# Kernel optimization log

Measured on AMD Instinct MI355X. Metric: run time of the kernel, lower is better.

The kernel has to match this reference:

```python
import jax, jax.numpy as jnp
import numpy as np

GRID = 7
NB = 2            # boxes per cell
NC = 20           # classes
IS = NB * 4       # start of confidence channels
D = NB * 5 + NC   # 30 channels per cell
B = 8192
L_BOX = 5.0       # threshold_box
L_NEG = 0.5       # threshold_conf_neg


def _bce(logits, target):
    # stable binary_cross_entropy_with_logits, elementwise (reduction handled by caller)
    return jnp.maximum(logits, 0.0) - logits * target + jnp.log1p(jnp.exp(-jnp.abs(logits)))


def _ltrb(xywh):
    xy, wh = xywh[..., :2], xywh[..., 2:4]
    return jnp.concatenate([xy - wh * 0.5, xy + wh * 0.5], axis=-1)


def _iou(a, b):
    lt = jnp.maximum(a[..., :2], b[..., :2])
    rb = jnp.minimum(a[..., 2:], b[..., 2:])
    wh = jnp.maximum(rb - lt, 0.0)
    inter = wh[..., 0] * wh[..., 1]
    area_a = (a[..., 2] - a[..., 0]) * (a[..., 3] - a[..., 1])
    area_b = (b[..., 2] - b[..., 0]) * (b[..., 3] - b[..., 1])
    return inter / (area_a + area_b - inter + 1e-7)


def _box_loss(pb, gb):
    # (x,y) MSE + (sqrt|w|, sqrt h) MSE, summed over the 4 coords -> shape = pb.shape[:-1]
    lxy = jnp.sum((pb[..., :2] - gb[..., :2]) ** 2, axis=-1)
    lwh = jnp.sum((jnp.sqrt(jnp.abs(pb[..., 2:4])) - jnp.sqrt(gb[..., 2:4])) ** 2, axis=-1)
    return lxy + lwh


def _forward(p, g):
    batch = p.shape[0]
    conf_g = g[..., IS]                    # [B,S,S] first gt confidence
    mask_pos = conf_g > 0
    mask_neg = conf_g == 0

    # positive-cell class loss (BCE with logits, sum)
    cls_cell = _bce(p[..., NB * 5:], g[..., NB * 5:]).sum(-1)
    loss_cls_pos = jnp.sum(jnp.where(mask_pos, cls_cell, 0.0))

    # negative-cell confidence loss vs zeros
    neg_cell = _bce(p[..., IS:IS + 2], 0.0).sum(-1)
    loss_conf_neg = jnp.sum(jnp.where(mask_neg, neg_cell, 0.0))

    # per-cell boxes: [B,S,S,NB,4]
    pbox = p[..., :IS].reshape(batch, GRID, GRID, NB, 4)
    gbox = g[..., :IS].reshape(batch, GRID, GRID, NB, 4)
    poff = jnp.concatenate([jax.nn.sigmoid(pbox[..., :2]), pbox[..., 2:]], axis=-1)

    # grid offsets: colrow_index = [col=ds2, row=ds1]; xy = (offxy + colrow) / grid
    row = jnp.broadcast_to(jnp.arange(GRID, dtype=p.dtype)[:, None], (GRID, GRID))
    col = jnp.broadcast_to(jnp.arange(GRID, dtype=p.dtype)[None, :], (GRID, GRID))
    cr = jnp.stack([col, row], axis=-1)[None, :, :, None, :]   # [1,S,S,1,2]

    # IoU matching is done under no_grad in the original -> stop_gradient
    poff_ng = jax.lax.stop_gradient(poff)
    p_ltrb = _ltrb(jnp.concatenate([(poff_ng[..., :2] + cr) / GRID, poff_ng[..., 2:]], -1))
    g_ltrb = _ltrb(jnp.concatenate([(gbox[..., :2] + cr) / GRID, gbox[..., 2:]], -1))
    ious = _iou(p_ltrb[..., :, None, :], g_ltrb[..., None, :, :])   # [B,S,S,NB,NB]
    ind = jnp.argmax(ious, axis=-2)                                  # best pbox per gbox, [B,S,S,NB]

    same_g = jnp.all(gbox[..., 0, :] == gbox[..., 1, :], axis=-1)
    same_ind = ind[..., 0] == ind[..., 1]

    gathered = jnp.take_along_axis(poff, ind[..., :, None], axis=-2)  # poff[ind]
    lossA = _box_loss(gathered[..., 0, :], gbox[..., 0, :])           # identical gt boxes
    lossB = _box_loss(poff, gbox).sum(-1)
    lossC = _box_loss(gathered, gbox).sum(-1)                          # distinct matches
    box_cell = jnp.where(same_g, lossA, jnp.where(same_ind, lossB, lossC))

    pconf = p[..., IS:IS + 2]
    confA = _bce(jnp.take_along_axis(pconf, ind[..., 1:2], axis=-1)[..., 0], 1.0)
    confBC = _bce(pconf, 1.0).sum(-1)
    conf_cell = jnp.where(same_g, confA, confBC)

    loss_box_pos = jnp.sum(jnp.where(mask_pos, box_cell, 0.0))
    loss_conf_pos = jnp.sum(jnp.where(mask_pos, conf_cell, 0.0))

    nb = jnp.asarray(batch, p.dtype)
    loss_box = L_BOX * loss_box_pos / nb
    loss_conf = (loss_conf_pos + L_NEG * loss_conf_neg) / nb
    loss_cls = loss_cls_pos / nb
    return loss_box + loss_conf + loss_cls


def setup_inputs() -> dict:
    key = jax.random.key(0)
    k1, k2, k3, k4 = jax.random.split(key, 4)
    p = jax.random.normal(k1, (B, GRID, GRID, D), dtype=jnp.float32)
    # both conf channels equal (mask semantics), class targets in [0,1]
    boxes = 0.05 + 0.9 * jax.random.uniform(k2, (B, GRID, GRID, IS), dtype=jnp.float32)
    conf = (jax.random.uniform(k3, (B, GRID, GRID, 1)) < 0.3).astype(jnp.float32)
    cls = jax.random.uniform(k4, (B, GRID, GRID, NC), dtype=jnp.float32)
    g = jnp.concatenate([boxes, conf, conf, cls], axis=-1)
    return {"p_yolo_ts": p, "g_yolo_ts": g}


def reference(p_yolo_ts, g_yolo_ts):
    return _forward(p_yolo_ts, g_yolo_ts)
```

## Files before the change

### kernel.cpp

```cpp
#include <hip/hip_runtime.h>
#include <math.h>

#define GRID_N 7
#define NB 2
#define NC 20
#define IS 8
#define DCH 30
#define BATCH 8192
#define NCELL (BATCH * GRID_N * GRID_N)
#define INV_GRID (1.0f / 7.0f)
#define INV_BATCH (1.0f / 8192.0f)

__device__ __forceinline__ float bce(float l, float t) {
    return fmaxf(l, 0.0f) - l * t + logf(1.0f + expf(-fabsf(l)));
}

__device__ __forceinline__ float box_loss(const float* pb, const float* gb) {
    float dx = pb[0] - gb[0];
    float dy = pb[1] - gb[1];
    float dw = sqrtf(fabsf(pb[2])) - sqrtf(gb[2]);
    float dh = sqrtf(fabsf(pb[3])) - sqrtf(gb[3]);
    return dx * dx + dy * dy + dw * dw + dh * dh;
}

__global__ __launch_bounds__(256) void yolo_loss_kernel(
        const float* __restrict__ p, const float* __restrict__ g,
        float* __restrict__ out) {
    const int cell = blockIdx.x * blockDim.x + threadIdx.x;
    float acc = 0.0f;

    if (cell < NCELL) {
        const int ij = cell % (GRID_N * GRID_N);
        const float fi = (float)(ij / GRID_N);
        const float fj = (float)(ij % GRID_N);

        float pv[DCH], gv[DCH];
        const float2* p2 = reinterpret_cast<const float2*>(p) + (long)cell * (DCH / 2);
        const float2* g2 = reinterpret_cast<const float2*>(g) + (long)cell * (DCH / 2);
        #pragma unroll
        for (int k = 0; k < DCH / 2; ++k) { float2 v = p2[k]; pv[2*k] = v.x; pv[2*k+1] = v.y; }
        #pragma unroll
        for (int k = 0; k < DCH / 2; ++k) { float2 v = g2[k]; gv[2*k] = v.x; gv[2*k+1] = v.y; }

        const float conf_g = gv[IS];

        if (conf_g == 0.0f) {
            acc = 0.5f * (bce(pv[IS], 0.0f) + bce(pv[IS + 1], 0.0f));
        } else if (conf_g > 0.0f) {
            float cls = 0.0f;
            #pragma unroll
            for (int c = 0; c < NC; ++c) cls += bce(pv[NB * 5 + c], gv[NB * 5 + c]);

            float po[NB][4];
            #pragma unroll
            for (int k = 0; k < NB; ++k) {
                po[k][0] = 1.0f / (1.0f + expf(-pv[4*k + 0]));
                po[k][1] = 1.0f / (1.0f + expf(-pv[4*k + 1]));
                po[k][2] = pv[4*k + 2];
                po[k][3] = pv[4*k + 3];
            }

            float pl[NB][4], gl[NB][4], pa[NB], ga[NB];
            #pragma unroll
            for (int k = 0; k < NB; ++k) {
                float cx = (po[k][0] + fj) * INV_GRID;
                float cy = (po[k][1] + fi) * INV_GRID;
                float w = po[k][2], h = po[k][3];
                pl[k][0] = cx - w * 0.5f; pl[k][1] = cy - h * 0.5f;
                pl[k][2] = cx + w * 0.5f; pl[k][3] = cy + h * 0.5f;
                pa[k] = (pl[k][2] - pl[k][0]) * (pl[k][3] - pl[k][1]);
            }
            #pragma unroll
            for (int m = 0; m < NB; ++m) {
                float cx = (gv[4*m + 0] + fj) * INV_GRID;
                float cy = (gv[4*m + 1] + fi) * INV_GRID;
                float w = gv[4*m + 2], h = gv[4*m + 3];
                gl[m][0] = cx - w * 0.5f; gl[m][1] = cy - h * 0.5f;
                gl[m][2] = cx + w * 0.5f; gl[m][3] = cy + h * 0.5f;
                ga[m] = (gl[m][2] - gl[m][0]) * (gl[m][3] - gl[m][1]);
            }

            int ind[NB];
            #pragma unroll
            for (int m = 0; m < NB; ++m) {
                float iou_km[NB];
                #pragma unroll
                for (int k = 0; k < NB; ++k) {
                    float ltx = fmaxf(pl[k][0], gl[m][0]);
                    float lty = fmaxf(pl[k][1], gl[m][1]);
                    float rbx = fminf(pl[k][2], gl[m][2]);
                    float rby = fminf(pl[k][3], gl[m][3]);
                    float w = fmaxf(rbx - ltx, 0.0f);
                    float h = fmaxf(rby - lty, 0.0f);
                    float inter = w * h;
                    iou_km[k] = inter / (pa[k] + ga[m] - inter + 1e-7f);
                }
                ind[m] = (iou_km[1] > iou_km[0]) ? 1 : 0;
            }

            float gth0[4], gth1[4];
            #pragma unroll
            for (int c = 0; c < 4; ++c) {
                gth0[c] = ind[0] ? po[1][c] : po[0][c];
                gth1[c] = ind[1] ? po[1][c] : po[0][c];
            }

            bool same_g = (gv[0] == gv[4]) && (gv[1] == gv[5]) &&
                          (gv[2] == gv[6]) && (gv[3] == gv[7]);
            bool same_ind = (ind[0] == ind[1]);

            float lossA = box_loss(gth0, &gv[0]);
            float lossB = box_loss(po[0], &gv[0]) + box_loss(po[1], &gv[4]);
            float lossC = box_loss(gth0, &gv[0]) + box_loss(gth1, &gv[4]);
            float box_cell = same_g ? lossA : (same_ind ? lossB : lossC);

            float pc0 = pv[IS], pc1 = pv[IS + 1];
            float confA = bce(ind[1] ? pc1 : pc0, 1.0f);
            float confBC = bce(pc0, 1.0f) + bce(pc1, 1.0f);
            float conf_cell = same_g ? confA : confBC;

            acc = 5.0f * box_cell + conf_cell + cls;
        }
    }

    #pragma unroll
    for (int off = 32; off > 0; off >>= 1) acc += __shfl_down(acc, off, 64);

    __shared__ float ws_red[4];
    const int lane = threadIdx.x & 63;
    const int wid = threadIdx.x >> 6;
    if (lane == 0) ws_red[wid] = acc;
    __syncthreads();
    if (threadIdx.x == 0) {
        float s = ws_red[0] + ws_red[1] + ws_red[2] + ws_red[3];
        atomicAdd(out, s * INV_BATCH);
    }
}

extern "C" void kernel_launch(void* const* d_in, const int* in_sizes, int n_in,
                              void* d_out, int out_size, void* d_ws, size_t ws_size,
                              hipStream_t stream) {
    const float* p = (const float*)d_in[0];
    const float* g = (const float*)d_in[1];
    float* out = (float*)d_out;

    hipMemsetAsync(out, 0, sizeof(float), stream);

    const int block = 256;
    const int grid = (NCELL + block - 1) / block;
    yolo_loss_kernel<<<grid, block, 0, stream>>>(p, g, out);
}
```

Measured before the change: 121.3 us.

## Stage cell tiles into LDS via coalesced global_load_lds before per-cell compute

```diff
diff --git a/kernel.cpp b/kernel.cpp
--- a/kernel.cpp
+++ b/kernel.cpp
@@ -11,6 +11,9 @@
 #define INV_GRID (1.0f / 7.0f)
 #define INV_BATCH (1.0f / 8192.0f)
 
+#define CELLS_PER_BLOCK 256
+#define F4_PER_BLOCK (CELLS_PER_BLOCK * DCH / 4)
+
 __device__ __forceinline__ float bce(float l, float t) {
     return fmaxf(l, 0.0f) - l * t + logf(1.0f + expf(-fabsf(l)));
 }
@@ -23,110 +26,137 @@
     return dx * dx + dy * dy + dw * dw + dh * dh;
 }
 
+__device__ __forceinline__ void load_lds16(const float4* gptr, float4* lptr) {
+    __builtin_amdgcn_global_load_lds(
+        (const __attribute__((address_space(1))) void*)(gptr),
+        (__attribute__((address_space(3))) void*)(lptr),
+        16, 0, 0);
+}
+
 __global__ __launch_bounds__(256) void yolo_loss_kernel(
         const float* __restrict__ p, const float* __restrict__ g,
         float* __restrict__ out) {
-    const int cell = blockIdx.x * blockDim.x + threadIdx.x;
+    __shared__ float sp[CELLS_PER_BLOCK * DCH];
+    __shared__ float sg[CELLS_PER_BLOCK * DCH];
+    __shared__ float ws_red[4];
+
+    const int tid = threadIdx.x;
+    const long blockCell = (long)blockIdx.x * CELLS_PER_BLOCK;
+
+    const float4* pB = reinterpret_cast<const float4*>(p + blockCell * DCH);
+    const float4* gB = reinterpret_cast<const float4*>(g + blockCell * DCH);
+    float4* sp4 = reinterpret_cast<float4*>(sp);
+    float4* sg4 = reinterpret_cast<float4*>(sg);
+
+    #pragma unroll
+    for (int k = 0; k < 7; ++k) {
+        load_lds16(pB + k * 256 + tid, sp4 + k * 256 + tid);
+        load_lds16(gB + k * 256 + tid, sg4 + k * 256 + tid);
+    }
+    if (tid < F4_PER_BLOCK - 7 * 256) {
+        load_lds16(pB + 7 * 256 + tid, sp4 + 7 * 256 + tid);
+        load_lds16(gB + 7 * 256 + tid, sg4 + 7 * 256 + tid);
+    }
+    __syncthreads();
+
+    const float* pv = sp + tid * DCH;
+    const float* gv = sg + tid * DCH;
+
+    const int cell = (int)blockCell + tid;
+    const int ij = cell % (GRID_N * GRID_N);
+    const float fi = (float)(ij / GRID_N);
+    const float fj = (float)(ij % GRID_N);
+
     float acc = 0.0f;
+    const float conf_g = gv[IS];
 
-    if (cell < NCELL) {
-        const int ij = cell % (GRID_N * GRID_N);
-        const float fi = (float)(ij / GRID_N);
-        const float fj = (float)(ij % GRID_N);
+    if (conf_g == 0.0f) {
+        acc = 0.5f * (bce(pv[IS], 0.0f) + bce(pv[IS + 1], 0.0f));
+    } else if (conf_g > 0.0f) {
+        float cls = 0.0f;
+        #pragma unroll
+        for (int c = 0; c < NC; ++c) cls += bce(pv[NB * 5 + c], gv[NB * 5 + c]);
 
-        float pv[DCH], gv[DCH];
-        const float2* p2 = reinterpret_cast<const float2*>(p) + (long)cell * (DCH / 2);
-        const float2* g2 = reinterpret_cast<const float2*>(g) + (long)cell * (DCH / 2);
+        float po[NB][4];
         #pragma unroll
-        for (int k = 0; k < DCH / 2; ++k) { float2 v = p2[k]; pv[2*k] = v.x; pv[2*k+1] = v.y; }
+        for (int k = 0; k < NB; ++k) {
+            po[k][0] = 1.0f / (1.0f + expf(-pv[4*k + 0]));
+            po[k][1] = 1.0f / (1.0f + expf(-pv[4*k + 1]));
+            po[k][2] = pv[4*k + 2];
+            po[k][3] = pv[4*k + 3];
+        }
+
+        float pl[NB][4], gl[NB][4], pa[NB], ga[NB];
+        float gbx[NB][4];
         #pragma unroll
-        for (int k = 0; k < DCH / 2; ++k) { float2 v = g2[k]; gv[2*k] = v.x; gv[2*k+1] = v.y; }
+        for (int m = 0; m < NB; ++m) {
+            gbx[m][0] = gv[4*m + 0]; gbx[m][1] = gv[4*m + 1];
+            gbx[m][2] = gv[4*m + 2]; gbx[m][3] = gv[4*m + 3];
+        }
+        #pragma unroll
+        for (int k = 0; k < NB; ++k) {
+            float cx = (po[k][0] + fj) * INV_GRID;
+            float cy = (po[k][1] + fi) * INV_GRID;
+            float w = po[k][2], h = po[k][3];
+            pl[k][0] = cx - w * 0.5f; pl[k][1] = cy - h * 0.5f;
+            pl[k][2] = cx + w * 0.5f; pl[k][3] = cy + h * 0.5f;
+            pa[k] = (pl[k][2] - pl[k][0]) * (pl[k][3] - pl[k][1]);
+        }
+        #pragma unroll
+        for (int m = 0; m < NB; ++m) {
+            float cx = (gbx[m][0] + fj) * INV_GRID;
+            float cy = (gbx[m][1] + fi) * INV_GRID;
+            float w = gbx[m][2], h = gbx[m][3];
+            gl[m][0] = cx - w * 0.5f; gl[m][1] = cy - h * 0.5f;
+            gl[m][2] = cx + w * 0.5f; gl[m][3] = cy + h * 0.5f;
+            ga[m] = (gl[m][2] - gl[m][0]) * (gl[m][3] - gl[m][1]);
+        }
 
-        const float conf_g = gv[IS];
-
-        if (conf_g == 0.0f) {
-            acc = 0.5f * (bce(pv[IS], 0.0f) + bce(pv[IS + 1], 0.0f));
-        } else if (conf_g > 0.0f) {
-            float cls = 0.0f;
-            #pragma unroll
-            for (int c = 0; c < NC; ++c) cls += bce(pv[NB * 5 + c], gv[NB * 5 + c]);
-
-            float po[NB][4];
+        int ind[NB];
+        #pragma unroll
+        for (int m = 0; m < NB; ++m) {
+            float iou_km[NB];
             #pragma unroll
             for (int k = 0; k < NB; ++k) {
-                po[k][0] = 1.0f / (1.0f + expf(-pv[4*k + 0]));
-                po[k][1] = 1.0f / (1.0f + expf(-pv[4*k + 1]));
-                po[k][2] = pv[4*k + 2];
-                po[k][3] = pv[4*k + 3];
+                float ltx = fmaxf(pl[k][0], gl[m][0]);
+                float lty = fmaxf(pl[k][1], gl[m][1]);
+                float rbx = fminf(pl[k][2], gl[m][2]);
+                float rby = fminf(pl[k][3], gl[m][3]);
+                float w = fmaxf(rbx - ltx, 0.0f);
+                float h = fmaxf(rby - lty, 0.0f);
+                float inter = w * h;
+                iou_km[k] = inter / (pa[k] + ga[m] - inter + 1e-7f);
             }
+            ind[m] = (iou_km[1] > iou_km[0]) ? 1 : 0;
+        }
 
-            float pl[NB][4], gl[NB][4], pa[NB], ga[NB];
-            #pragma unroll
-            for (int k = 0; k < NB; ++k) {
-                float cx = (po[k][0] + fj) * INV_GRID;
-                float cy = (po[k][1] + fi) * INV_GRID;
-                float w = po[k][2], h = po[k][3];
-                pl[k][0] = cx - w * 0.5f; pl[k][1] = cy - h * 0.5f;
-                pl[k][2] = cx + w * 0.5f; pl[k][3] = cy + h * 0.5f;
-                pa[k] = (pl[k][2] - pl[k][0]) * (pl[k][3] - pl[k][1]);
-            }
-            #pragma unroll
-            for (int m = 0; m < NB; ++m) {
-                float cx = (gv[4*m + 0] + fj) * INV_GRID;
-                float cy = (gv[4*m + 1] + fi) * INV_GRID;
-                float w = gv[4*m + 2], h = gv[4*m + 3];
-                gl[m][0] = cx - w * 0.5f; gl[m][1] = cy - h * 0.5f;
-                gl[m][2] = cx + w * 0.5f; gl[m][3] = cy + h * 0.5f;
-                ga[m] = (gl[m][2] - gl[m][0]) * (gl[m][3] - gl[m][1]);
-            }
+        float gth0[4], gth1[4];
+        #pragma unroll
+        for (int c = 0; c < 4; ++c) {
+            gth0[c] = ind[0] ? po[1][c] : po[0][c];
+            gth1[c] = ind[1] ? po[1][c] : po[0][c];
+        }
 
-            int ind[NB];
-            #pragma unroll
-            for (int m = 0; m < NB; ++m) {
-                float iou_km[NB];
-                #pragma unroll
-                for (int k = 0; k < NB; ++k) {
-                    float ltx = fmaxf(pl[k][0], gl[m][0]);
-                    float lty = fmaxf(pl[k][1], gl[m][1]);
-                    float rbx = fminf(pl[k][2], gl[m][2]);
-                    float rby = fminf(pl[k][3], gl[m][3]);
-                    float w = fmaxf(rbx - ltx, 0.0f);
-                    float h = fmaxf(rby - lty, 0.0f);
-                    float inter = w * h;
-                    iou_km[k] = inter / (pa[k] + ga[m] - inter + 1e-7f);
-                }
-                ind[m] = (iou_km[1] > iou_km[0]) ? 1 : 0;
-            }
+        bool same_g = (gbx[0][0] == gbx[1][0]) && (gbx[0][1] == gbx[1][1]) &&
+                      (gbx[0][2] == gbx[1][2]) && (gbx[0][3] == gbx[1][3]);
+        bool same_ind = (ind[0] == ind[1]);
 
-            float gth0[4], gth1[4];
-            #pragma unroll
-            for (int c = 0; c < 4; ++c) {
-                gth0[c] = ind[0] ? po[1][c] : po[0][c];
-                gth1[c] = ind[1] ? po[1][c] : po[0][c];
-            }
+        float lossA = box_loss(gth0, gbx[0]);
+        float lossB = box_loss(po[0], gbx[0]) + box_loss(po[1], gbx[1]);
+        float lossC = box_loss(gth0, gbx[0]) + box_loss(gth1, gbx[1]);
+        float box_cell = same_g ? lossA : (same_ind ? lossB : lossC);
 
-            bool same_g = (gv[0] == gv[4]) && (gv[1] == gv[5]) &&
-                          (gv[2] == gv[6]) && (gv[3] == gv[7]);
-            bool same_ind = (ind[0] == ind[1]);
+        float pc0 = pv[IS], pc1 = pv[IS + 1];
+        float confA = bce(ind[1] ? pc1 : pc0, 1.0f);
+        float confBC = bce(pc0, 1.0f) + bce(pc1, 1.0f);
+        float conf_cell = same_g ? confA : confBC;
 
-            float lossA = box_loss(gth0, &gv[0]);
-            float lossB = box_loss(po[0], &gv[0]) + box_loss(po[1], &gv[4]);
-            float lossC = box_loss(gth0, &gv[0]) + box_loss(gth1, &gv[4]);
-            float box_cell = same_g ? lossA : (same_ind ? lossB : lossC);
-
-            float pc0 = pv[IS], pc1 = pv[IS + 1];
-            float confA = bce(ind[1] ? pc1 : pc0, 1.0f);
-            float confBC = bce(pc0, 1.0f) + bce(pc1, 1.0f);
-            float conf_cell = same_g ? confA : confBC;
-
-            acc = 5.0f * box_cell + conf_cell + cls;
-        }
+        acc = 5.0f * box_cell + conf_cell + cls;
     }
 
     #pragma unroll
     for (int off = 32; off > 0; off >>= 1) acc += __shfl_down(acc, off, 64);
 
-    __shared__ float ws_red[4];
     const int lane = threadIdx.x & 63;
     const int wid = threadIdx.x >> 6;
     if (lane == 0) ws_red[wid] = acc;
@@ -147,6 +177,6 @@
     hipMemsetAsync(out, 0, sizeof(float), stream);
 
     const int block = 256;
-    const int grid = (NCELL + block - 1) / block;
+    const int grid = NCELL / CELLS_PER_BLOCK;
     yolo_loss_kernel<<<grid, block, 0, stream>>>(p, g, out);
 }
```

Result: no change. 119.2 us (-1.7%).
